# Optimization experiments

Measured on AMD Instinct MI355X. Metric: run time of the kernel, lower is better.

## Reference

```python
import jax, jax.numpy as jnp
import numpy as np
from jax import lax

NEG_SLOPE = 0.2  # cfg.negativeSlope
CHANS = [1, 4, 8, 16, 32, 64]
B = 1024


def lrelu(x):
    return jnp.where(x >= 0, x, NEG_SLOPE * x)


def conv3d(x, w):
    # x: [B,C,D,H,W], w: [O,I,3,3,3], stride 1, padding 1 (SAME)
    return lax.conv_general_dilated(
        x, w, window_strides=(1, 1, 1), padding='SAME',
        dimension_numbers=('NCDHW', 'OIDHW', 'NCDHW'))


def maxpool2(x):
    return lax.reduce_window(x, -jnp.inf, lax.max,
                             (1, 1, 2, 2, 2), (1, 1, 2, 2, 2), 'VALID')


def setup_inputs() -> dict:
    key = jax.random.key(0)
    ks = jax.random.split(key, 12)
    inp = {'voxel': jax.random.uniform(ks[0], (B, 1, 32, 32, 32), jnp.float32)}
    for i in range(5):
        fan_in = CHANS[i] * 27
        inp[f'conv_w{i+1}'] = jax.random.normal(
            ks[1 + i], (CHANS[i + 1], CHANS[i], 3, 3, 3), jnp.float32) / np.sqrt(fan_in)
        inp[f'conv_b{i+1}'] = jnp.zeros((CHANS[i + 1],), jnp.float32)
    # 6 parallel heads (3 plane SP + 3 quaternion RQ), stacked on axis 0
    dims = [(64, 32), (32, 16), (16, 4)]
    for j, (fi, fo) in enumerate(dims):
        inp[f'W{j+1}'] = jax.random.normal(ks[6 + j], (6, fi, fo), jnp.float32) / np.sqrt(fi)
        inp[f'b{j+1}'] = jnp.zeros((6, fo), jnp.float32)
    return inp


def reference(voxel, conv_w1, conv_b1, conv_w2, conv_b2, conv_w3, conv_b3,
              conv_w4, conv_b4, conv_w5, conv_b5, W1, b1, W2, b2, W3, b3):
    x = voxel
    for w, b in ((conv_w1, conv_b1), (conv_w2, conv_b2), (conv_w3, conv_b3),
                 (conv_w4, conv_b4), (conv_w5, conv_b5)):
        # torch order: conv -> maxpool -> LeakyReLU
        x = lrelu(maxpool2(conv3d(x, w) + b[None, :, None, None, None]))
    feat = x.reshape(x.shape[0], 64)  # [B,64] (spatial collapsed to 1^3)
    # 6 heads batched: [B,64] x [6,64,32] -> [B,6,32] -> [B,6,16] -> [B,6,4]
    h = lrelu(jnp.einsum('bf,hfo->bho', feat, W1) + b1)
    h = lrelu(jnp.einsum('bho,hop->bhp', h, W2) + b2)
    h = lrelu(jnp.einsum('bhp,hpq->bhq', h, W3) + b3)
    # unitize: divide by L2 norm over the 4-vector (torch.norm dim=1 of [B,4])
    out = h / jnp.linalg.norm(h, axis=-1, keepdims=True)
    return out
```

## Files before the change

kernel.cpp:

```cpp
#include <hip/hip_runtime.h>
#include <math.h>

#define NEG_SLOPE 0.2f

typedef _Float16 half2_t __attribute__((ext_vector_type(2)));

__device__ __forceinline__ float lrelu(float x) {
    return fmaxf(x, NEG_SLOPE * x);
}

__device__ __forceinline__ float fdot2(half2_t a, half2_t b, float c) {
#if __has_builtin(__builtin_amdgcn_fdot2)
    return __builtin_amdgcn_fdot2(a, b, c, false);
#else
    return c + (float)a.x * (float)b.x + (float)a.y * (float)b.y;
#endif
}

__device__ __forceinline__ half2_t as_h2(uint u) {
    union { uint u; half2_t h; } c; c.u = u; return c.h;
}

constexpr int clog2(int n) { return (n <= 1) ? 0 : 1 + clog2(n / 2); }

template<int CI, int CO, int S, int ZT, int PZT, int CPT, int BPB>
__global__ __launch_bounds__(256, 4) void conv_pool_f32h(
    const float* __restrict__ in,
    const float* __restrict__ w,
    const float* __restrict__ bias,
    half2_t* __restrict__ out,
    int B)
{
    constexpr int SP    = S / 2;
    constexpr int ZD    = 2 * ZT + 2;
    constexpr int YS    = S + 2;
    constexpr int XOFF  = 5;
    constexpr int XR    = S + 8;
    constexpr int PLANE = YS * XR;
    constexpr int NPAIR = BPB * CI * ZD;
    constexpr int LDS_N = NPAIR * PLANE;
    constexpr int NOG   = CO / CPT;
    constexpr int NZB   = ZT / PZT;
    constexpr int NPOS  = NZB * SP * SP;
    constexpr int NSLAB = SP / ZT;
    static_assert(BPB * NOG * NPOS == 256, "thread mapping must cover block");
    static_assert((LDS_N & 3) == 0, "float4 zero");
    static_assert((CPT & 1) == 0, "pack pairs");

    __shared__ __align__(16) float sm[LDS_N];

    const int t     = threadIdx.x;
    const int zslab = blockIdx.x & (NSLAB - 1);
    const int b0    = (blockIdx.x >> clog2(NSLAB)) * BPB;
    const int zp0   = zslab * ZT;
    const int gz0   = 2 * zp0 - 1;

    {
        float4* s4 = (float4*)sm;
        constexpr int N4 = LDS_N / 4;
#pragma unroll
        for (int i = 0; i < (N4 + 255) / 256; ++i) {
            const int k = t + i * 256;
            if (k < N4) s4[k] = make_float4(0.f, 0.f, 0.f, 0.f);
        }
    }
    __syncthreads();

    {
        constexpr int CHUNKS = S / 4;
        constexpr int PJOBS  = S * CHUNKS;
        constexpr int PPI    = 256 / PJOBS;
        constexpr int FITER  = NPAIR / PPI;
        static_assert(FITER * PPI == NPAIR, "fill covers planes exactly");
        const int idx  = t & (PJOBS - 1);
        const int poff = t >> clog2(PJOBS);
        const int cc   = idx & (CHUNKS - 1);
        const int yy   = idx >> clog2(CHUNKS);
#pragma unroll
        for (int it = 0; it < FITER; ++it) {
            const int plane = it * PPI + poff;
            const int z     = plane % ZD;
            const int bci   = plane / ZD;
            const int gz    = gz0 + z;
            if ((unsigned)gz < (unsigned)S) {
                const float4 v = *(const float4*)&in[
                    ((long)(b0 * CI + bci) * S + gz) * (S * S) + yy * S + 4 * cc];
                float* sp = &sm[(plane * YS + (yy + 1)) * XR + XOFF + 4 * cc];
                sp[0] = v.x; sp[1] = v.y; sp[2] = v.z; sp[3] = v.w;
            }
        }
    }
    __syncthreads();

    const int pos = t & (NPOS - 1);
    const int og  = __builtin_amdgcn_readfirstlane(
                        (t >> clog2(NPOS)) & (NOG - 1));
    const int bl  = __builtin_amdgcn_readfirstlane(
                        t >> clog2(NPOS * NOG));
    const int xp  = pos & (SP - 1);
    const int yp  = (pos >> clog2(SP)) & (SP - 1);
    const int zb  = pos >> (2 * clog2(SP));

#pragma unroll
    for (int zi = 0; zi < PZT; ++zi) {
        const int zl = zb * PZT + zi;
        float acc[CPT][8];
#pragma unroll
        for (int oo = 0; oo < CPT; ++oo)
#pragma unroll
            for (int p = 0; p < 8; ++p) acc[oo][p] = 0.f;

#pragma unroll 1
        for (int ci = 0; ci < CI; ++ci) {
            const float* sp_ = &sm[((bl * CI + ci) * ZD + 2 * zl) * PLANE +
                                   (2 * yp) * XR + 2 * xp + (XOFF - 1)];
#pragma unroll
            for (int dz = 0; dz < 4; ++dz) {
                float v[4][4];
#pragma unroll
                for (int dy = 0; dy < 4; ++dy) {
                    const float2 q0 = *(const float2*)&sp_[dz * PLANE + dy * XR];
                    const float2 q1 = *(const float2*)&sp_[dz * PLANE + dy * XR + 2];
                    v[dy][0] = q0.x; v[dy][1] = q0.y;
                    v[dy][2] = q1.x; v[dy][3] = q1.y;
                }
#pragma unroll
                for (int kz = 0; kz < 3; ++kz) {
                    const int pz = dz - kz;
                    if (pz >= 0 && pz < 2) {
#pragma unroll
                        for (int oo = 0; oo < CPT; ++oo) {
                            const float* wp = w +
                                (long)((og * CPT + oo) * CI + ci) * 27 + kz * 9;
#pragma unroll
                            for (int ky = 0; ky < 3; ++ky)
#pragma unroll
                                for (int kx = 0; kx < 3; ++kx) {
                                    const float wv = wp[ky * 3 + kx];
#pragma unroll
                                    for (int py = 0; py < 2; ++py)
#pragma unroll
                                        for (int px = 0; px < 2; ++px)
                                            acc[oo][pz * 4 + py * 2 + px] +=
                                                v[py + ky][px + kx] * wv;
                                }
                        }
                    }
                }
            }
        }

#pragma unroll
        for (int oo = 0; oo < CPT; oo += 2) {
            const int o = og * CPT + oo;
            float m0 = acc[oo][0], m1 = acc[oo + 1][0];
#pragma unroll
            for (int p = 1; p < 8; ++p) {
                m0 = fmaxf(m0, acc[oo][p]);
                m1 = fmaxf(m1, acc[oo + 1][p]);
            }
            half2_t hv;
            hv.x = (_Float16)lrelu(m0 + bias[o]);
            hv.y = (_Float16)lrelu(m1 + bias[o + 1]);
            out[(long)((b0 + bl) * (CO / 2) + (o >> 1)) * (SP * SP * SP) +
                ((zp0 + zl) * SP + yp) * SP + xp] = hv;
        }
    }
}

template<int CIH, int CO, int S, int ZT, int PZT, int CPT, int BPB>
__global__ __launch_bounds__(256, 4) void conv_pool_h2(
    const half2_t* __restrict__ in,
    const uint*   __restrict__ wh,
    const float*  __restrict__ bias,
    half2_t* __restrict__ out,
    int B)
{
    constexpr int SP    = S / 2;
    constexpr int ZD    = 2 * ZT + 2;
    constexpr int YS    = S + 2;
    constexpr int XOFF  = 3;
    constexpr int XR    = S + 6;
    constexpr int PLANE = YS * XR;
    constexpr int NPAIR = BPB * CIH * ZD;
    constexpr int LDS_N = NPAIR * PLANE;
    constexpr int NOG   = CO / CPT;
    constexpr int NZB   = ZT / PZT;
    constexpr int NPOS  = NZB * SP * SP;
    constexpr int NSLAB = SP / ZT;
    static_assert(BPB * NOG * NPOS == 256, "thread mapping must cover block");
    static_assert((LDS_N & 3) == 0, "uint4 zero");
    static_assert((CPT & 1) == 0, "pack pairs");

    __shared__ __align__(16) uint sm[LDS_N];
    const uint* inu = (const uint*)in;

    const int t     = threadIdx.x;
    const int zslab = blockIdx.x & (NSLAB - 1);
    const int b0    = (blockIdx.x >> clog2(NSLAB)) * BPB;
    const int zp0   = zslab * ZT;
    const int gz0   = 2 * zp0 - 1;

    {
        uint4* s4 = (uint4*)sm;
        constexpr int N4 = LDS_N / 4;
#pragma unroll
        for (int i = 0; i < (N4 + 255) / 256; ++i) {
            const int k = t + i * 256;
            if (k < N4) s4[k] = make_uint4(0, 0, 0, 0);
        }
    }
    __syncthreads();

    {
        constexpr int CH    = S / 2;
        constexpr int PJOBS = S * CH;
        constexpr int ITERS = NPAIR * PJOBS / 256;
        static_assert(ITERS * 256 == NPAIR * PJOBS, "exact fill");
#pragma unroll
        for (int it = 0; it < ITERS; ++it) {
            const int i     = t + it * 256;
            const int idx   = i & (PJOBS - 1);
            const int plane = i >> clog2(PJOBS);
            const int cc    = idx & (CH - 1);
            const int yy    = idx >> clog2(CH);
            const int z     = plane % ZD;
            const int bci   = plane / ZD;
            const int gz    = gz0 + z;
            if ((unsigned)gz < (unsigned)S) {
                const uint2 v = *(const uint2*)&inu[
                    ((long)(b0 * CIH + bci) * S + gz) * (S * S) + yy * S + 2 * cc];
                uint* sp = &sm[(plane * YS + yy + 1) * XR + XOFF + 2 * cc];
                sp[0] = v.x; sp[1] = v.y;
            }
        }
    }
    __syncthreads();

    const int pos = t & (NPOS - 1);
    const int og  = __builtin_amdgcn_readfirstlane(
                        (t >> clog2(NPOS)) & (NOG - 1));
    const int bl  = __builtin_amdgcn_readfirstlane(
                        t >> clog2(NPOS * NOG));
    const int xp  = pos & (SP - 1);
    const int yp  = (pos >> clog2(SP)) & (SP - 1);
    const int zb  = pos >> (2 * clog2(SP));

#pragma unroll
    for (int zi = 0; zi < PZT; ++zi) {
        const int zl = zb * PZT + zi;
        float acc[CPT][8];
#pragma unroll
        for (int oo = 0; oo < CPT; ++oo)
#pragma unroll
            for (int p = 0; p < 8; ++p) acc[oo][p] = 0.f;

#pragma unroll 1
        for (int cp = 0; cp < CIH; ++cp) {
            const uint* sp_ = &sm[((bl * CIH + cp) * ZD + 2 * zl) * PLANE +
                                  (2 * yp) * XR + 2 * xp + (XOFF - 1)];
#pragma unroll
            for (int dz = 0; dz < 4; ++dz) {
                half2_t v[4][4];
#pragma unroll
                for (int dy = 0; dy < 4; ++dy) {
                    const uint2 q0 = *(const uint2*)&sp_[dz * PLANE + dy * XR];
                    const uint2 q1 = *(const uint2*)&sp_[dz * PLANE + dy * XR + 2];
                    v[dy][0] = as_h2(q0.x); v[dy][1] = as_h2(q0.y);
                    v[dy][2] = as_h2(q1.x); v[dy][3] = as_h2(q1.y);
                }
#pragma unroll
                for (int kz = 0; kz < 3; ++kz) {
                    const int pz = dz - kz;
                    if (pz >= 0 && pz < 2) {
#pragma unroll
                        for (int oo = 0; oo < CPT; ++oo) {
                            const uint* wp = wh +
                                (long)((og * CPT + oo) * CIH + cp) * 27 + kz * 9;
#pragma unroll
                            for (int ky = 0; ky < 3; ++ky)
#pragma unroll
                                for (int kx = 0; kx < 3; ++kx) {
                                    const half2_t wv = as_h2(wp[ky * 3 + kx]);
#pragma unroll
                                    for (int py = 0; py < 2; ++py)
#pragma unroll
                                        for (int px = 0; px < 2; ++px)
                                            acc[oo][pz * 4 + py * 2 + px] =
                                                fdot2(v[py + ky][px + kx], wv,
                                                      acc[oo][pz * 4 + py * 2 + px]);
                                }
                        }
                    }
                }
            }
        }

#pragma unroll
        for (int oo = 0; oo < CPT; oo += 2) {
            const int o = og * CPT + oo;
            float m0 = acc[oo][0], m1 = acc[oo + 1][0];
#pragma unroll
            for (int p = 1; p < 8; ++p) {
                m0 = fmaxf(m0, acc[oo][p]);
                m1 = fmaxf(m1, acc[oo + 1][p]);
            }
            half2_t hv;
            hv.x = (_Float16)lrelu(m0 + bias[o]);
            hv.y = (_Float16)lrelu(m1 + bias[o + 1]);
            out[(long)((b0 + bl) * (CO / 2) + (o >> 1)) * (SP * SP * SP) +
                ((zp0 + zl) * SP + yp) * SP + xp] = hv;
        }
    }
}

__global__ __launch_bounds__(256, 4) void tail_fused2(
    const uint*  __restrict__ in,
    const uint*  __restrict__ wh3,
    const uint*  __restrict__ wh4,
    const uint*  __restrict__ wh5,
    const float* __restrict__ cb3, const float* __restrict__ cb4,
    const float* __restrict__ cb5,
    const float* __restrict__ W1, const float* __restrict__ fb1,
    const float* __restrict__ W2, const float* __restrict__ fb2,
    const float* __restrict__ W3, const float* __restrict__ fb3,
    float* __restrict__ out)
{
    constexpr int S3IN  = 0;
    constexpr int S3OUT = 4800;
    constexpr int S4OUT = 6528;
    constexpr int FEAT  = 7552;
    constexpr int H1O   = 7616;
    constexpr int H2O   = 7808;
    constexpr int H3O   = 7904;
    constexpr int LDS_N = 7936;

    __shared__ __align__(16) uint sm[LDS_N];
    float* smf = (float*)sm;
    _Float16* s3h = (_Float16*)(sm + S3OUT);
    _Float16* s4h = (_Float16*)(sm + S4OUT);

    const int t = threadIdx.x;
    const int b = blockIdx.x;

    {
        uint4* s4 = (uint4*)sm;
#pragma unroll
        for (int i = 0; i < 8; ++i) {
            const int k = t + i * 256;
            if (k < LDS_N / 4) s4[k] = make_uint4(0, 0, 0, 0);
        }
    }
    __syncthreads();

#pragma unroll
    for (int it = 0; it < 4; ++it) {
        const int i  = t + it * 256;
        const int xc = i & 3;
        const int yy = (i >> 2) & 7;
        const int zz = (i >> 5) & 7;
        const int cp = i >> 8;
        const uint2 v = *(const uint2*)&in[
            ((long)b * 4 + cp) * 512 + (zz * 8 + yy) * 8 + 2 * xc];
        uint* sp = &sm[S3IN + cp * 1200 + (zz + 1) * 120 + (yy + 1) * 12 +
                       3 + 2 * xc];
        sp[0] = v.x; sp[1] = v.y;
    }
    __syncthreads();

    {
        const int pos = t & 63;
        const int cog = __builtin_amdgcn_readfirstlane(t >> 6);
        const int xp = pos & 3;
        const int yp = (pos >> 2) & 3;
        const int zp = pos >> 4;

        float acc[4][8];
#pragma unroll
        for (int oo = 0; oo < 4; ++oo)
#pragma unroll
            for (int p = 0; p < 8; ++p) acc[oo][p] = 0.f;

#pragma unroll 1
        for (int cp = 0; cp < 4; ++cp) {
            const uint* base = &sm[S3IN + cp * 1200 + 2 * zp * 120 +
                                   2 * yp * 12 + 2 * xp + 2];
#pragma unroll
            for (int dz = 0; dz < 4; ++dz) {
                half2_t v[4][4];
#pragma unroll
                for (int dy = 0; dy < 4; ++dy) {
                    const uint2 q0 = *(const uint2*)&base[dz * 120 + dy * 12];
                    const uint2 q1 = *(const uint2*)&base[dz * 120 + dy * 12 + 2];
                    v[dy][0] = as_h2(q0.x); v[dy][1] = as_h2(q0.y);
                    v[dy][2] = as_h2(q1.x); v[dy][3] = as_h2(q1.y);
                }
#pragma unroll
                for (int kz = 0; kz < 3; ++kz) {
                    const int pz = dz - kz;
                    if (pz >= 0 && pz < 2) {
#pragma unroll
                        for (int oo = 0; oo < 4; ++oo) {
                            const uint* wp = &wh3[((cog * 4 + oo) * 4 + cp) * 27 +
                                                  kz * 9];
#pragma unroll
                            for (int ky = 0; ky < 3; ++ky)
#pragma unroll
                                for (int kx = 0; kx < 3; ++kx) {
                                    const half2_t wv = as_h2(wp[ky * 3 + kx]);
#pragma unroll
                                    for (int py = 0; py < 2; ++py)
#pragma unroll
                                        for (int px = 0; px < 2; ++px)
                                            acc[oo][pz * 4 + py * 2 + px] =
                                                fdot2(v[py + ky][px + kx], wv,
                                                      acc[oo][pz * 4 + py * 2 + px]);
                                }
                        }
                    }
                }
            }
        }
        const int hbase = (((zp + 1) * 6 + (yp + 1)) * 6 + (xp + 1)) << 4;
#pragma unroll
        for (int oo = 0; oo < 4; ++oo) {
            const int co = cog * 4 + oo;
            float m = acc[oo][0];
#pragma unroll
            for (int p = 1; p < 8; ++p) m = fmaxf(m, acc[oo][p]);
            s3h[hbase + co] = (_Float16)lrelu(m + cb3[co]);
        }
    }
    __syncthreads();

    {
        const int co = t >> 3;
        const int pos = t & 7;
        const int xp = pos & 1;
        const int yp = (pos >> 1) & 1;
        const int zp = pos >> 2;
        const uint* vbase = &sm[S3OUT + (((2 * zp * 6 + 2 * yp) * 6 + 2 * xp) << 3)];
        float acc[8];
#pragma unroll
        for (int p = 0; p < 8; ++p) acc[p] = 0.f;
#pragma unroll 1
        for (int c = 0; c < 8; ++c) {
            const uint* wp = &wh4[(co * 8 + c) * 27];
#pragma unroll
            for (int dz = 0; dz < 4; ++dz) {
                half2_t v[4][4];
#pragma unroll
                for (int dy = 0; dy < 4; ++dy)
#pragma unroll
                    for (int dx = 0; dx < 4; ++dx)
                        v[dy][dx] = as_h2(vbase[(((dz * 6 + dy) * 6 + dx) << 3) + c]);
#pragma unroll
                for (int kz = 0; kz < 3; ++kz) {
                    const int pz = dz - kz;
                    if (pz >= 0 && pz < 2) {
#pragma unroll
                        for (int ky = 0; ky < 3; ++ky)
#pragma unroll
                            for (int kx = 0; kx < 3; ++kx) {
                                const half2_t wv = as_h2(wp[kz * 9 + ky * 3 + kx]);
#pragma unroll
                                for (int py = 0; py < 2; ++py)
#pragma unroll
                                    for (int px = 0; px < 2; ++px)
                                        acc[pz * 4 + py * 2 + px] =
                                            fdot2(v[py + ky][px + kx], wv,
                                                  acc[pz * 4 + py * 2 + px]);
                            }
                    }
                }
            }
        }
        float m = acc[0];
#pragma unroll
        for (int p = 1; p < 8; ++p) m = fmaxf(m, acc[p]);
        s4h[((((zp + 1) * 4 + (yp + 1)) * 4 + (xp + 1)) << 5) + co] =
            (_Float16)lrelu(m + cb4[co]);
    }
    __syncthreads();

    {
        const int co = t & 63;
        const int cq = __builtin_amdgcn_readfirstlane(t >> 6);
        float acc[8];
#pragma unroll
        for (int p = 0; p < 8; ++p) acc[p] = 0.f;
#pragma unroll 1
        for (int ci = 0; ci < 4; ++ci) {
            const int c = cq * 4 + ci;
            const uint* wp = &wh5[(co * 16 + c) * 27];
#pragma unroll
            for (int dz = 0; dz < 4; ++dz) {
                half2_t v[4][4];
#pragma unroll
                for (int dy = 0; dy < 4; ++dy)
#pragma unroll
                    for (int dx = 0; dx < 4; ++dx)
                        v[dy][dx] = as_h2(sm[S4OUT +
                            (((dz * 4 + dy) * 4 + dx) << 4) + c]);
#pragma unroll
                for (int kz = 0; kz < 3; ++kz) {
                    const int pz = dz - kz;
                    if (pz >= 0 && pz < 2) {
#pragma unroll
                        for (int ky = 0; ky < 3; ++ky)
#pragma unroll
                            for (int kx = 0; kx < 3; ++kx) {
                                const half2_t wv = as_h2(wp[kz * 9 + ky * 3 + kx]);
#pragma unroll
                                for (int py = 0; py < 2; ++py)
#pragma unroll
                                    for (int px = 0; px < 2; ++px)
                                        acc[pz * 4 + py * 2 + px] =
                                            fdot2(v[py + ky][px + kx], wv,
                                                  acc[pz * 4 + py * 2 + px]);
                            }
                    }
                }
            }
        }
#pragma unroll
        for (int p = 0; p < 8; ++p)
            smf[(cq * 64 + co) * 9 + p] = acc[p];
    }
    __syncthreads();

    if (t < 64) {
        float acc[8];
#pragma unroll
        for (int p = 0; p < 8; ++p)
            acc[p] = smf[t * 9 + p] + smf[(64 + t) * 9 + p] +
                     smf[(128 + t) * 9 + p] + smf[(192 + t) * 9 + p];
        float m = acc[0];
#pragma unroll
        for (int p = 1; p < 8; ++p) m = fmaxf(m, acc[p]);
        smf[FEAT + t] = lrelu(m + cb5[t]);
    }
    __syncthreads();

    if (t < 192) {
        const int j = t & 31;
        const int h = t >> 5;
        float s = fb1[h * 32 + j];
#pragma unroll
        for (int k = 0; k < 64; ++k)
            s += smf[FEAT + k] * W1[(h * 64 + k) * 32 + j];
        smf[H1O + h * 32 + j] = lrelu(s);
    }
    __syncthreads();

    if (t < 96) {
        const int j = t & 15;
        const int h = t >> 4;
        float s = fb2[h * 16 + j];
#pragma unroll
        for (int k = 0; k < 32; ++k)
            s += smf[H1O + h * 32 + k] * W2[(h * 32 + k) * 16 + j];
        smf[H2O + h * 16 + j] = lrelu(s);
    }
    __syncthreads();

    if (t < 24) {
        const int j = t & 3;
        const int h = t >> 2;
        float s = fb3[h * 4 + j];
#pragma unroll
        for (int k = 0; k < 16; ++k)
            s += smf[H2O + h * 16 + k] * W3[(h * 16 + k) * 4 + j];
        smf[H3O + h * 4 + j] = lrelu(s);
    }
    __syncthreads();

    if (t < 24) {
        const int q = t & 3;
        const int h = t >> 2;
        const float x0 = smf[H3O + h * 4 + 0];
        const float x1 = smf[H3O + h * 4 + 1];
        const float x2 = smf[H3O + h * 4 + 2];
        const float x3 = smf[H3O + h * 4 + 3];
        const float inv = 1.f / sqrtf(x0 * x0 + x1 * x1 + x2 * x2 + x3 * x3);
        out[(b * 6 + h) * 4 + q] = smf[H3O + h * 4 + q] * inv;
    }
}

__device__ __forceinline__ void pack_one(int i, const float* w, uint* h,
                                         int CO, int CI)
{
    const int CIH = CI / 2;
    const int n = CO * CIH * 27;
    if (i < n) {
        const int tap = i % 27;
        const int r   = i / 27;
        const int cp  = r % CIH;
        const int co  = r / CIH;
        const float* s = w + ((co * CI + 2 * cp) * 27 + tap);
        union { uint u; half2_t v; } c;
        c.v.x = (_Float16)s[0];
        c.v.y = (_Float16)s[27];
        h[i] = c.u;
    }
}

__global__ __launch_bounds__(256) void pack_weights(
    const float* w2, const float* w3, const float* w4, const float* w5,
    uint* h2, uint* h3, uint* h4, uint* h5)
{
    const int i = blockIdx.x * 256 + threadIdx.x;
    pack_one(i, w2, h2, 8, 4);
    pack_one(i, w3, h3, 16, 8);
    pack_one(i, w4, h4, 32, 16);
    pack_one(i, w5, h5, 64, 32);
}

extern "C" void kernel_launch(void* const* d_in, const int* in_sizes, int n_in,
                              void* d_out, int out_size, void* d_ws, size_t ws_size,
                              hipStream_t stream)
{
    const float* voxel = (const float*)d_in[0];
    const float* cw1 = (const float*)d_in[1];  const float* cb1 = (const float*)d_in[2];
    const float* cw2 = (const float*)d_in[3];  const float* cb2 = (const float*)d_in[4];
    const float* cw3 = (const float*)d_in[5];  const float* cb3 = (const float*)d_in[6];
    const float* cw4 = (const float*)d_in[7];  const float* cb4 = (const float*)d_in[8];
    const float* cw5 = (const float*)d_in[9];  const float* cb5 = (const float*)d_in[10];
    const float* W1  = (const float*)d_in[11]; const float* b1  = (const float*)d_in[12];
    const float* W2  = (const float*)d_in[13]; const float* b2  = (const float*)d_in[14];
    const float* W3  = (const float*)d_in[15]; const float* b3  = (const float*)d_in[16];
    float* out = (float*)d_out;

    const int B = 1024;
    uint* buf1h = (uint*)d_ws;
    uint* buf2h = buf1h + 8388608;
    uint* wh2   = buf2h + 2097152;
    uint* wh3   = wh2 + 432;
    uint* wh4   = wh3 + 1728;
    uint* wh5   = wh4 + 6912;

    pack_weights<<<108, 256, 0, stream>>>(cw2, cw3, cw4, cw5, wh2, wh3, wh4, wh5);

    conv_pool_f32h<1, 4, 32, 2, 2, 4, 1><<<1024 * 8, 256, 0, stream>>>(
        voxel, cw1, cb1, (half2_t*)buf1h, B);
    conv_pool_h2<2, 8, 16, 2, 2, 4, 2><<<512 * 4, 256, 0, stream>>>(
        (const half2_t*)buf1h, wh2, cb2, (half2_t*)buf2h, B);
    tail_fused2<<<1024, 256, 0, stream>>>(
        buf2h, wh3, wh4, wh5, cb3, cb4, cb5,
        W1, b1, W2, b2, W3, b3, out);
}
```

Baseline: 432.2 us.

## Share LDS input rows across z-pooled outputs and retune layer-2 conv tiling

Both conv+pool kernels now walk the z slab once per input channel and feed each loaded 4x4 input row set to every pooled z-output that uses it. Before, each pooled z row reloaded its own 4 planes, so overlapping planes were read twice. This keeps PZT*CPT*8 accumulators live at once instead of CPT*8, which raises register pressure. The layer-2 launch also drops to CPT=2 and BPB=1 with twice the blocks, and launch bounds go up to 6 waves to recover occupancy.

Measured after the change: 512.7 us. +18.6%, slower.

```diff
diff --git a/kernel.cpp b/kernel.cpp
--- a/kernel.cpp
+++ b/kernel.cpp
@@ -101,63 +101,71 @@
     const int yp  = (pos >> clog2(SP)) & (SP - 1);
     const int zb  = pos >> (2 * clog2(SP));
 
-#pragma unroll
-    for (int zi = 0; zi < PZT; ++zi) {
-        const int zl = zb * PZT + zi;
-        float acc[CPT][8];
+    float acc[PZT][CPT][8];
+#pragma unroll
+    for (int zi = 0; zi < PZT; ++zi)
 #pragma unroll
         for (int oo = 0; oo < CPT; ++oo)
 #pragma unroll
-            for (int p = 0; p < 8; ++p) acc[oo][p] = 0.f;
+            for (int p = 0; p < 8; ++p) acc[zi][oo][p] = 0.f;
 
 #pragma unroll 1
-        for (int ci = 0; ci < CI; ++ci) {
-            const float* sp_ = &sm[((bl * CI + ci) * ZD + 2 * zl) * PLANE +
-                                   (2 * yp) * XR + 2 * xp + (XOFF - 1)];
-#pragma unroll
-            for (int dz = 0; dz < 4; ++dz) {
-                float v[4][4];
-#pragma unroll
-                for (int dy = 0; dy < 4; ++dy) {
-                    const float2 q0 = *(const float2*)&sp_[dz * PLANE + dy * XR];
-                    const float2 q1 = *(const float2*)&sp_[dz * PLANE + dy * XR + 2];
-                    v[dy][0] = q0.x; v[dy][1] = q0.y;
-                    v[dy][2] = q1.x; v[dy][3] = q1.y;
-                }
-#pragma unroll
-                for (int kz = 0; kz < 3; ++kz) {
-                    const int pz = dz - kz;
-                    if (pz >= 0 && pz < 2) {
-#pragma unroll
-                        for (int oo = 0; oo < CPT; ++oo) {
-                            const float* wp = w +
-                                (long)((og * CPT + oo) * CI + ci) * 27 + kz * 9;
-#pragma unroll
-                            for (int ky = 0; ky < 3; ++ky)
-#pragma unroll
-                                for (int kx = 0; kx < 3; ++kx) {
-                                    const float wv = wp[ky * 3 + kx];
-#pragma unroll
-                                    for (int py = 0; py < 2; ++py)
-#pragma unroll
-                                        for (int px = 0; px < 2; ++px)
-                                            acc[oo][pz * 4 + py * 2 + px] +=
-                                                v[py + ky][px + kx] * wv;
-                                }
+    for (int ci = 0; ci < CI; ++ci) {
+        const float* sp_ = &sm[((bl * CI + ci) * ZD + 2 * zb * PZT) * PLANE +
+                               (2 * yp) * XR + 2 * xp + (XOFF - 1)];
+#pragma unroll
+        for (int dz = 0; dz < 2 * PZT + 2; ++dz) {
+            float v[4][4];
+#pragma unroll
+            for (int dy = 0; dy < 4; ++dy) {
+                const float2 q0 = *(const float2*)&sp_[dz * PLANE + dy * XR];
+                const float2 q1 = *(const float2*)&sp_[dz * PLANE + dy * XR + 2];
+                v[dy][0] = q0.x; v[dy][1] = q0.y;
+                v[dy][2] = q1.x; v[dy][3] = q1.y;
+            }
+#pragma unroll
+            for (int zi = 0; zi < PZT; ++zi) {
+                const int dzl = dz - 2 * zi;
+                if (dzl >= 0 && dzl < 4) {
+#pragma unroll
+                    for (int kz = 0; kz < 3; ++kz) {
+                        const int pz = dzl - kz;
+                        if (pz >= 0 && pz < 2) {
+#pragma unroll
+                            for (int oo = 0; oo < CPT; ++oo) {
+                                const float* wp = w +
+                                    (long)((og * CPT + oo) * CI + ci) * 27 + kz * 9;
+#pragma unroll
+                                for (int ky = 0; ky < 3; ++ky)
+#pragma unroll
+                                    for (int kx = 0; kx < 3; ++kx) {
+                                        const float wv = wp[ky * 3 + kx];
+#pragma unroll
+                                        for (int py = 0; py < 2; ++py)
+#pragma unroll
+                                            for (int px = 0; px < 2; ++px)
+                                                acc[zi][oo][pz * 4 + py * 2 + px] +=
+                                                    v[py + ky][px + kx] * wv;
+                                    }
+                            }
                         }
                     }
                 }
             }
         }
-
+    }
+
+#pragma unroll
+    for (int zi = 0; zi < PZT; ++zi) {
+        const int zl = zb * PZT + zi;
 #pragma unroll
         for (int oo = 0; oo < CPT; oo += 2) {
             const int o = og * CPT + oo;
-            float m0 = acc[oo][0], m1 = acc[oo + 1][0];
+            float m0 = acc[zi][oo][0], m1 = acc[zi][oo + 1][0];
 #pragma unroll
             for (int p = 1; p < 8; ++p) {
-                m0 = fmaxf(m0, acc[oo][p]);
-                m1 = fmaxf(m1, acc[oo + 1][p]);
+                m0 = fmaxf(m0, acc[zi][oo][p]);
+                m1 = fmaxf(m1, acc[zi][oo + 1][p]);
             }
             half2_t hv;
             hv.x = (_Float16)lrelu(m0 + bias[o]);
@@ -169,7 +177,7 @@
 }
 
 template<int CIH, int CO, int S, int ZT, int PZT, int CPT, int BPB>
-__global__ __launch_bounds__(256, 4) void conv_pool_h2(
+__global__ __launch_bounds__(256, 6) void conv_pool_h2(
     const half2_t* __restrict__ in,
     const uint*   __restrict__ wh,
     const float*  __restrict__ bias,
@@ -246,64 +254,72 @@
     const int yp  = (pos >> clog2(SP)) & (SP - 1);
     const int zb  = pos >> (2 * clog2(SP));
 
-#pragma unroll
-    for (int zi = 0; zi < PZT; ++zi) {
-        const int zl = zb * PZT + zi;
-        float acc[CPT][8];
+    float acc[PZT][CPT][8];
+#pragma unroll
+    for (int zi = 0; zi < PZT; ++zi)
 #pragma unroll
         for (int oo = 0; oo < CPT; ++oo)
 #pragma unroll
-            for (int p = 0; p < 8; ++p) acc[oo][p] = 0.f;
+            for (int p = 0; p < 8; ++p) acc[zi][oo][p] = 0.f;
 
 #pragma unroll 1
-        for (int cp = 0; cp < CIH; ++cp) {
-            const uint* sp_ = &sm[((bl * CIH + cp) * ZD + 2 * zl) * PLANE +
-                                  (2 * yp) * XR + 2 * xp + (XOFF - 1)];
-#pragma unroll
-            for (int dz = 0; dz < 4; ++dz) {
-                half2_t v[4][4];
-#pragma unroll
-                for (int dy = 0; dy < 4; ++dy) {
-                    const uint2 q0 = *(const uint2*)&sp_[dz * PLANE + dy * XR];
-                    const uint2 q1 = *(const uint2*)&sp_[dz * PLANE + dy * XR + 2];
-                    v[dy][0] = as_h2(q0.x); v[dy][1] = as_h2(q0.y);
-                    v[dy][2] = as_h2(q1.x); v[dy][3] = as_h2(q1.y);
-                }
-#pragma unroll
-                for (int kz = 0; kz < 3; ++kz) {
-                    const int pz = dz - kz;
-                    if (pz >= 0 && pz < 2) {
-#pragma unroll
-                        for (int oo = 0; oo < CPT; ++oo) {
-                            const uint* wp = wh +
-                                (long)((og * CPT + oo) * CIH + cp) * 27 + kz * 9;
-#pragma unroll
-                            for (int ky = 0; ky < 3; ++ky)
-#pragma unroll
-                                for (int kx = 0; kx < 3; ++kx) {
-                                    const half2_t wv = as_h2(wp[ky * 3 + kx]);
-#pragma unroll
-                                    for (int py = 0; py < 2; ++py)
-#pragma unroll
-                                        for (int px = 0; px < 2; ++px)
-                                            acc[oo][pz * 4 + py * 2 + px] =
-                                                fdot2(v[py + ky][px + kx], wv,
-                                                      acc[oo][pz * 4 + py * 2 + px]);
-                                }
+    for (int cp = 0; cp < CIH; ++cp) {
+        const uint* sp_ = &sm[((bl * CIH + cp) * ZD + 2 * zb * PZT) * PLANE +
+                              (2 * yp) * XR + 2 * xp + (XOFF - 1)];
+#pragma unroll
+        for (int dz = 0; dz < 2 * PZT + 2; ++dz) {
+            half2_t v[4][4];
+#pragma unroll
+            for (int dy = 0; dy < 4; ++dy) {
+                const uint2 q0 = *(const uint2*)&sp_[dz * PLANE + dy * XR];
+                const uint2 q1 = *(const uint2*)&sp_[dz * PLANE + dy * XR + 2];
+                v[dy][0] = as_h2(q0.x); v[dy][1] = as_h2(q0.y);
+                v[dy][2] = as_h2(q1.x); v[dy][3] = as_h2(q1.y);
+            }
+#pragma unroll
+            for (int zi = 0; zi < PZT; ++zi) {
+                const int dzl = dz - 2 * zi;
+                if (dzl >= 0 && dzl < 4) {
+#pragma unroll
+                    for (int kz = 0; kz < 3; ++kz) {
+                        const int pz = dzl - kz;
+                        if (pz >= 0 && pz < 2) {
+#pragma unroll
+                            for (int oo = 0; oo < CPT; ++oo) {
+                                const uint* wp = wh +
+                                    (long)((og * CPT + oo) * CIH + cp) * 27 + kz * 9;
+#pragma unroll
+                                for (int ky = 0; ky < 3; ++ky)
+#pragma unroll
+                                    for (int kx = 0; kx < 3; ++kx) {
+                                        const half2_t wv = as_h2(wp[ky * 3 + kx]);
+#pragma unroll
+                                        for (int py = 0; py < 2; ++py)
+#pragma unroll
+                                            for (int px = 0; px < 2; ++px)
+                                                acc[zi][oo][pz * 4 + py * 2 + px] =
+                                                    fdot2(v[py + ky][px + kx], wv,
+                                                          acc[zi][oo][pz * 4 + py * 2 + px]);
+                                    }
+                            }
                         }
                     }
                 }
             }
         }
-
+    }
+
+#pragma unroll
+    for (int zi = 0; zi < PZT; ++zi) {
+        const int zl = zb * PZT + zi;
 #pragma unroll
         for (int oo = 0; oo < CPT; oo += 2) {
             const int o = og * CPT + oo;
-            float m0 = acc[oo][0], m1 = acc[oo + 1][0];
+            float m0 = acc[zi][oo][0], m1 = acc[zi][oo + 1][0];
 #pragma unroll
             for (int p = 1; p < 8; ++p) {
-                m0 = fmaxf(m0, acc[oo][p]);
-                m1 = fmaxf(m1, acc[oo + 1][p]);
+                m0 = fmaxf(m0, acc[zi][oo][p]);
+                m1 = fmaxf(m1, acc[zi][oo + 1][p]);
             }
             half2_t hv;
             hv.x = (_Float16)lrelu(m0 + bias[o]);
@@ -643,7 +659,7 @@
 
     conv_pool_f32h<1, 4, 32, 2, 2, 4, 1><<<1024 * 8, 256, 0, stream>>>(
         voxel, cw1, cb1, (half2_t*)buf1h, B);
-    conv_pool_h2<2, 8, 16, 2, 2, 4, 2><<<512 * 4, 256, 0, stream>>>(
+    conv_pool_h2<2, 8, 16, 2, 2, 2, 1><<<1024 * 4, 256, 0, stream>>>(
         (const half2_t*)buf1h, wh2, cb2, (half2_t*)buf2h, B);
     tail_fused2<<<1024, 256, 0, stream>>>(
         buf2h, wh3, wh4, wh5, cb3, cb4, cb5,
```
